# Performance work log

Measured on AMD Instinct MI355X. Metric: run time of the kernel, lower is better.

## Reference

```python
import jax, jax.numpy as jnp
import numpy as np
from jax import lax

H = W = 496
K = 5            # gabor kernel size
WIN = 16         # window_size
STRIDE = 16
PATCH = 32
GAMMA = 0.5
PSI = np.pi / 2
THETAS = np.array([np.pi/8, np.pi/4, 3*np.pi/8, np.pi/2, 5*np.pi/8, 6*np.pi/8, 7*np.pi/8, np.pi], dtype=np.float32)


def setup_inputs() -> dict:
    key = jax.random.key(0)
    k1, k2, k3 = jax.random.split(key, 3)
    img = jax.random.normal(k1, (1, 1, H, W), dtype=jnp.float32)
    sigmas = jax.random.uniform(k2, (1, 3), dtype=jnp.float32) * 10.0   # nn.Parameter(rand*10)
    lambdas = jax.random.uniform(k3, (1, 3), dtype=jnp.float32) * np.pi  # nn.Parameter(rand*pi)
    return {"img": img, "sigmas": sigmas, "lambdas": lambdas}


def _gabor_bank(sigmas, lambdas):
    # axes: (sigma, lambda, theta, ky, kx)
    idx = jnp.arange(K, dtype=jnp.float32) - (K - 1) / 2.0
    sig = sigmas[0][:, None, None, None, None]          # [3,1,1,1,1]
    lam = lambdas[0][None, :, None, None, None]         # [1,3,1,1,1]
    th = jnp.asarray(THETAS)[None, None, :, None, None] # [1,1,8,1,1]
    y = idx[None, None, None, :, None]
    x = idx[None, None, None, None, :]
    sigma_x = sig
    sigma_y = sig / GAMMA
    sin_t, cos_t = jnp.sin(th), jnp.cos(th)
    y_theta = -x * sin_t + y * cos_t
    x_theta = x * cos_t + y * sin_t
    gb = jnp.exp(-0.5 * (x_theta**2 / sigma_x**2 + y_theta**2 / sigma_y**2)) \
         * jnp.cos(2.0 * np.pi * x_theta / lam + PSI)
    return gb.reshape(-1, 1, K, K)  # [72,1,5,5]


def reference(img, sigmas, lambdas):
    gb = _gabor_bank(sigmas, lambdas)
    res = lax.conv_general_dilated(
        img, gb, window_strides=(1, 1), padding=[(K // 2, K // 2)] * 2,
        dimension_numbers=("NCHW", "OIHW", "NCHW"))          # [1,72,H,W]
    res = res.reshape(1, 9, 8, H, W).max(axis=2)              # max over 8 thetas -> [1,9,H,W]
    out = res[0]                                              # [9,H,W]

    # find_maxima: per-channel threshold at 5*mean, zero below (torch.nn.Threshold)
    mean = out.mean(axis=(1, 2), keepdims=True)
    thr = jnp.where(out > mean * 5.0, out, 0.0)

    nw = H // STRIDE                                          # 31
    windows = thr.reshape(9, nw, WIN, nw, WIN).transpose(0, 1, 3, 2, 4).reshape(9, nw * nw, WIN * WIN)
    is_max = jnp.argmax(windows, axis=2) == (WIN * WIN) // 2  # [9, 961]

    w_idx = jnp.arange(nw * nw)
    rows = w_idx // nw * STRIDE + WIN // 2
    cols = w_idx % nw * STRIDE + WIN // 2

    # describe: zero-pad by 16, gather 32x32 patch at each candidate keypoint for every channel
    pad = jnp.pad(out, ((0, 0), (16, 16), (16, 16)))
    pr = rows[:, None, None] + jnp.arange(PATCH)[None, :, None]   # [961,32,1]
    pc = cols[:, None, None] + jnp.arange(PATCH)[None, None, :]   # [961,1,32]
    patches = pad[:, pr, pc]                                      # [9,961,32,32]

    # keep patches only for detected keypoints with nonzero content (original skips zero patches)
    valid_kp = jnp.any(is_max, axis=0)                            # [961]
    nonzero = jnp.any(patches != 0, axis=(2, 3))                  # [9,961]
    mask = (valid_kp[None, :] & nonzero).astype(patches.dtype)
    patches = patches * mask[:, :, None, None]
    return patches
```

## Files before the change

kernel.cpp:

```cpp
#include <hip/hip_runtime.h>
#include <math.h>

#define HH 496
#define WW 496
#define HWSZ (HH*WW)
#define NW 31
#define NWIN (NW*NW)

typedef float nf4 __attribute__((ext_vector_type(4)));

__constant__ float c_thetas[8] = {
    0.39269908169872414f, 0.7853981633974483f, 1.1780972450961724f,
    1.5707963267948966f,  1.9634954084936207f, 2.356194490192345f,
    2.748893571891069f,   3.141592653589793f};

__global__ void bank_kernel(const float* __restrict__ sigmas,
                            const float* __restrict__ lambdas,
                            float* __restrict__ filt,
                            float* __restrict__ meanacc) {
    int idx = threadIdx.x + blockIdx.x * blockDim.x;
    if (idx >= 1800) {
        if (idx < 1809) meanacc[(idx - 1800) * 16] = 0.0f;
        return;
    }
    int f = idx / 25, k = idx % 25;
    int dy = k / 5, dx = k % 5;
    int s = f / 24, rem = f % 24, l = rem / 8, t = rem % 8;
    float sig = sigmas[s], lam = lambdas[l], th = c_thetas[t];
    float y = (float)dy - 2.0f, x = (float)dx - 2.0f;
    float st = sinf(th), ct = cosf(th);
    float yt = -x * st + y * ct;
    float xt =  x * ct + y * st;
    float sx2 = sig * sig;
    float sy2 = 4.0f * sig * sig;
    float g = expf(-0.5f * (xt * xt / sx2 + yt * yt / sy2)) *
              cosf(6.28318530717958647692f * xt / lam + 1.5707963267948966f);
    filt[k * 72 + f] = g;
}

#define FMAS(FP, P) \
    a0  = fmaf(P, (FP)[0],  a0);  a1  = fmaf(P, (FP)[1],  a1);  \
    a2  = fmaf(P, (FP)[2],  a2);  a3  = fmaf(P, (FP)[3],  a3);  \
    a4  = fmaf(P, (FP)[4],  a4);  a5  = fmaf(P, (FP)[5],  a5);  \
    a6  = fmaf(P, (FP)[6],  a6);  a7  = fmaf(P, (FP)[7],  a7);  \
    a8  = fmaf(P, (FP)[8],  a8);  a9  = fmaf(P, (FP)[9],  a9);  \
    a10 = fmaf(P, (FP)[10], a10); a11 = fmaf(P, (FP)[11], a11); \
    a12 = fmaf(P, (FP)[12], a12); a13 = fmaf(P, (FP)[13], a13); \
    a14 = fmaf(P, (FP)[14], a14); a15 = fmaf(P, (FP)[15], a15); \
    a16 = fmaf(P, (FP)[16], a16); a17 = fmaf(P, (FP)[17], a17); \
    a18 = fmaf(P, (FP)[18], a18); a19 = fmaf(P, (FP)[19], a19); \
    a20 = fmaf(P, (FP)[20], a20); a21 = fmaf(P, (FP)[21], a21); \
    a22 = fmaf(P, (FP)[22], a22); a23 = fmaf(P, (FP)[23], a23);

#define STEP(K) { const float* fp = fbase + (K)*72; FMAS(fp, p##K) }

#define ALLSTEPS \
    STEP(0)  STEP(1)  STEP(2)  STEP(3)  STEP(4)  \
    STEP(5)  STEP(6)  STEP(7)  STEP(8)  STEP(9)  \
    STEP(10) STEP(11) STEP(12) STEP(13) STEP(14) \
    STEP(15) STEP(16) STEP(17) STEP(18) STEP(19) \
    STEP(20) STEP(21) STEP(22) STEP(23) STEP(24)

__global__ __launch_bounds__(256) void conv_kernel(
    const float* __restrict__ img, const float* __restrict__ filt,
    float* __restrict__ out, float* __restrict__ meanacc) {
    __shared__ float tile[20 * 20];
    __shared__ float red[4][3];
    int tid = threadIdx.x;
    int tx = tid & 15, ty = tid >> 4;
    int bx = blockIdx.x, by = blockIdx.y, cg = blockIdx.z;

    for (int i = tid; i < 400; i += 256) {
        int tY = i / 20, tX = i % 20;
        int gy = by * 16 + tY - 2, gx = bx * 16 + tX - 2;
        float v = 0.0f;
        if (gy >= 0 && gy < HH && gx >= 0 && gx < WW) v = img[gy * WW + gx];
        tile[i] = v;
    }
    __syncthreads();

    int tbase = ty * 20 + tx;
    float p0  = tile[tbase +  0], p1  = tile[tbase +  1], p2  = tile[tbase +  2],
          p3  = tile[tbase +  3], p4  = tile[tbase +  4];
    float p5  = tile[tbase + 20], p6  = tile[tbase + 21], p7  = tile[tbase + 22],
          p8  = tile[tbase + 23], p9  = tile[tbase + 24];
    float p10 = tile[tbase + 40], p11 = tile[tbase + 41], p12 = tile[tbase + 42],
          p13 = tile[tbase + 43], p14 = tile[tbase + 44];
    float p15 = tile[tbase + 60], p16 = tile[tbase + 61], p17 = tile[tbase + 62],
          p18 = tile[tbase + 63], p19 = tile[tbase + 64];
    float p20 = tile[tbase + 80], p21 = tile[tbase + 81], p22 = tile[tbase + 82],
          p23 = tile[tbase + 83], p24 = tile[tbase + 84];

    float a0=0,a1=0,a2=0,a3=0,a4=0,a5=0,a6=0,a7=0,a8=0,a9=0,a10=0,a11=0,
          a12=0,a13=0,a14=0,a15=0,a16=0,a17=0,a18=0,a19=0,a20=0,a21=0,a22=0,a23=0;
    const float* fbase = filt + cg * 24;

    ALLSTEPS

    int y = by * 16 + ty, x = bx * 16 + tx;

    float m0 = fmaxf(fmaxf(fmaxf(a0,a1),fmaxf(a2,a3)),fmaxf(fmaxf(a4,a5),fmaxf(a6,a7)));
    float m1 = fmaxf(fmaxf(fmaxf(a8,a9),fmaxf(a10,a11)),fmaxf(fmaxf(a12,a13),fmaxf(a14,a15)));
    float m2 = fmaxf(fmaxf(fmaxf(a16,a17),fmaxf(a18,a19)),fmaxf(fmaxf(a20,a21),fmaxf(a22,a23)));

    out[(cg * 3 + 0) * HWSZ + y * WW + x] = m0;
    out[(cg * 3 + 1) * HWSZ + y * WW + x] = m1;
    out[(cg * 3 + 2) * HWSZ + y * WW + x] = m2;

#define RED(CC, MV) { \
        float s = MV; \
        s += __shfl_down(s, 32, 64); s += __shfl_down(s, 16, 64); \
        s += __shfl_down(s,  8, 64); s += __shfl_down(s,  4, 64); \
        s += __shfl_down(s,  2, 64); s += __shfl_down(s,  1, 64); \
        if ((tid & 63) == 0) red[tid >> 6][CC] = s; }
    RED(0, m0) RED(1, m1) RED(2, m2)
    __syncthreads();
    if (tid < 3)
        atomicAdd(&meanacc[(cg * 3 + tid) * 16],
                  red[0][tid] + red[1][tid] + red[2][tid] + red[3][tid]);
}

__global__ __launch_bounds__(256) void patch_kernel(
    const float* __restrict__ out, const float* __restrict__ meanacc,
    float* __restrict__ dst) {
    int w = blockIdx.x;
    int r = w / NW, cl = w % NW;
    int tid = threadIdx.x;
    __shared__ int lds_and[4];
    __shared__ int lds_or[4];

    int wy = tid >> 4, wx = tid & 15;
    int rowbase = (r * 16 + wy) * WW + cl * 16 + wx;
    int cbase   = (r * 16 + 8) * WW + cl * 16;
    int okmask = 0;
#pragma unroll
    for (int c = 0; c < 9; c++) {
        float m5 = meanacc[c * 16] * (5.0f / (float)HWSZ);
        float v  = out[c * HWSZ + rowbase];
        float vc = out[c * HWSZ + cbase];
        float thr  = (v  > m5) ? v  : 0.0f;
        float thrc = (vc > m5) ? vc : 0.0f;
        bool ok = (tid < 128) ? (thr < thrc) : (thr <= thrc);
        okmask |= (ok ? 1 : 0) << c;
    }
#pragma unroll
    for (int off = 1; off < 64; off <<= 1) okmask &= __shfl_xor(okmask, off, 64);
    if ((tid & 63) == 0) lds_and[tid >> 6] = okmask;

    int i = tid >> 3;
    int jg = (tid & 7) << 2;
    int row = r * 16 + i - 8;
    int col = cl * 16 + jg - 8;
    bool inb = (row >= 0 && row < HH && col >= 0 && col + 3 < WW);
    size_t pbase = (size_t)row * WW + col;
    int nzmask = 0;
    nf4 p0, p1, p2, p3, p4, p5, p6, p7, p8;
#define LOADP(C, V) { \
        V = (nf4){0.f, 0.f, 0.f, 0.f}; \
        if (inb) V = *(const nf4*)(out + (size_t)(C) * HWSZ + pbase); \
        if (V.x != 0.f || V.y != 0.f || V.z != 0.f || V.w != 0.f) nzmask |= 1 << (C); }
    LOADP(0,p0) LOADP(1,p1) LOADP(2,p2) LOADP(3,p3) LOADP(4,p4)
    LOADP(5,p5) LOADP(6,p6) LOADP(7,p7) LOADP(8,p8)

#pragma unroll
    for (int off = 1; off < 64; off <<= 1) nzmask |= __shfl_xor(nzmask, off, 64);
    if ((tid & 63) == 0) lds_or[tid >> 6] = nzmask;
    __syncthreads();

    int am = lds_and[0] & lds_and[1] & lds_and[2] & lds_and[3];
    int om = lds_or[0] | lds_or[1] | lds_or[2] | lds_or[3];
    bool valid = (am != 0);

    size_t dbase = (size_t)w * 1024 + i * 32 + jg;
#define STOREP(C, V) { \
        float mk = (valid && ((om >> (C)) & 1)) ? 1.0f : 0.0f; \
        V *= mk; \
        __builtin_nontemporal_store(V, (nf4*)(dst + (size_t)(C) * NWIN * 1024 + dbase)); }
    STOREP(0,p0) STOREP(1,p1) STOREP(2,p2) STOREP(3,p3) STOREP(4,p4)
    STOREP(5,p5) STOREP(6,p6) STOREP(7,p7) STOREP(8,p8)
}

extern "C" void kernel_launch(void* const* d_in, const int* in_sizes, int n_in,
                              void* d_out, int out_size, void* d_ws, size_t ws_size,
                              hipStream_t stream) {
    const float* img     = (const float*)d_in[0];
    const float* sigmas  = (const float*)d_in[1];
    const float* lambdas = (const float*)d_in[2];
    float* ws = (float*)d_ws;
    float* filt    = ws;
    float* meanacc = ws + 2048;
    float* outb    = ws + 4096;

    bank_kernel<<<8, 256, 0, stream>>>(sigmas, lambdas, filt, meanacc);
    conv_kernel<<<dim3(NW, NW, 3), 256, 0, stream>>>(img, filt, outb, meanacc);
    patch_kernel<<<NWIN, 256, 0, stream>>>(outb, meanacc, (float*)d_out);
}
```

Measured before the change: 121.6 us.

## Compute per-window max statistics in conv kernel to simplify keypoint test

The conv kernel now also reduces each 16x16 window to a max over pixels before the centre, a max over pixels after it, and the centre value, and writes these to a small workspace array. The patch kernel decides whether a keypoint is valid from these three values and the channel mean, instead of reloading the whole window per channel and doing a ballot-style reduction. This removes 9 window reads and a cross-wave reduction from the patch kernel. In exchange the conv kernel does an extra max reduction and more shared-memory work. The threshold-then-argmax semantics now rely on comparing the centre against the other maxima without zeroing sub-threshold values, which may behave differently in edge cases.

After: 123.9 us. Within noise of the previous version (+1.9%).

```diff
diff --git a/kernel.cpp b/kernel.cpp
--- a/kernel.cpp
+++ b/kernel.cpp
@@ -1,5 +1,6 @@
 #include <hip/hip_runtime.h>
 #include <math.h>
+#include <float.h>
 
 #define HH 496
 #define WW 496
@@ -63,9 +64,12 @@
 
 __global__ __launch_bounds__(256) void conv_kernel(
     const float* __restrict__ img, const float* __restrict__ filt,
-    float* __restrict__ out, float* __restrict__ meanacc) {
+    float* __restrict__ out, float* __restrict__ meanacc,
+    float* __restrict__ winfo) {
     __shared__ float tile[20 * 20];
     __shared__ float red[4][3];
+    __shared__ float wmax[4][3];
+    __shared__ float cen[3];
     int tid = threadIdx.x;
     int tx = tid & 15, ty = tid >> 4;
     int bx = blockIdx.x, by = blockIdx.y, cg = blockIdx.z;
@@ -107,45 +111,47 @@
     out[(cg * 3 + 1) * HWSZ + y * WW + x] = m1;
     out[(cg * 3 + 2) * HWSZ + y * WW + x] = m2;
 
-#define RED(CC, MV) { \
+#define REDBOTH(CC, MV) { \
         float s = MV; \
         s += __shfl_down(s, 32, 64); s += __shfl_down(s, 16, 64); \
         s += __shfl_down(s,  8, 64); s += __shfl_down(s,  4, 64); \
         s += __shfl_down(s,  2, 64); s += __shfl_down(s,  1, 64); \
-        if ((tid & 63) == 0) red[tid >> 6][CC] = s; }
-    RED(0, m0) RED(1, m1) RED(2, m2)
+        float q = (tid == 128) ? -FLT_MAX : MV; \
+        q = fmaxf(q, __shfl_down(q, 32, 64)); q = fmaxf(q, __shfl_down(q, 16, 64)); \
+        q = fmaxf(q, __shfl_down(q,  8, 64)); q = fmaxf(q, __shfl_down(q,  4, 64)); \
+        q = fmaxf(q, __shfl_down(q,  2, 64)); q = fmaxf(q, __shfl_down(q,  1, 64)); \
+        if ((tid & 63) == 0) { red[tid >> 6][CC] = s; wmax[tid >> 6][CC] = q; } \
+        if (tid == 128) cen[CC] = MV; }
+    REDBOTH(0, m0) REDBOTH(1, m1) REDBOTH(2, m2)
     __syncthreads();
-    if (tid < 3)
+    int w = by * NW + bx;
+    if (tid < 3) {
         atomicAdd(&meanacc[(cg * 3 + tid) * 16],
                   red[0][tid] + red[1][tid] + red[2][tid] + red[3][tid]);
+        int c = cg * 3 + tid;
+        winfo[0 * 9 * NWIN + c * NWIN + w] = fmaxf(wmax[0][tid], wmax[1][tid]);
+        winfo[1 * 9 * NWIN + c * NWIN + w] = fmaxf(wmax[2][tid], wmax[3][tid]);
+        winfo[2 * 9 * NWIN + c * NWIN + w] = cen[tid];
+    }
 }
 
 __global__ __launch_bounds__(256) void patch_kernel(
     const float* __restrict__ out, const float* __restrict__ meanacc,
-    float* __restrict__ dst) {
+    const float* __restrict__ winfo, float* __restrict__ dst) {
     int w = blockIdx.x;
     int r = w / NW, cl = w % NW;
     int tid = threadIdx.x;
-    __shared__ int lds_and[4];
     __shared__ int lds_or[4];
 
-    int wy = tid >> 4, wx = tid & 15;
-    int rowbase = (r * 16 + wy) * WW + cl * 16 + wx;
-    int cbase   = (r * 16 + 8) * WW + cl * 16;
-    int okmask = 0;
+    bool valid = false;
 #pragma unroll
     for (int c = 0; c < 9; c++) {
-        float m5 = meanacc[c * 16] * (5.0f / (float)HWSZ);
-        float v  = out[c * HWSZ + rowbase];
-        float vc = out[c * HWSZ + cbase];
-        float thr  = (v  > m5) ? v  : 0.0f;
-        float thrc = (vc > m5) ? vc : 0.0f;
-        bool ok = (tid < 128) ? (thr < thrc) : (thr <= thrc);
-        okmask |= (ok ? 1 : 0) << c;
-    }
-#pragma unroll
-    for (int off = 1; off < 64; off <<= 1) okmask &= __shfl_xor(okmask, off, 64);
-    if ((tid & 63) == 0) lds_and[tid >> 6] = okmask;
+        float m5  = meanacc[c * 16] * (5.0f / (float)HWSZ);
+        float me  = winfo[0 * 9 * NWIN + c * NWIN + w];
+        float mlt = winfo[1 * 9 * NWIN + c * NWIN + w];
+        float ce  = winfo[2 * 9 * NWIN + c * NWIN + w];
+        if (ce > m5 && ce > me && ce >= mlt) valid = true;
+    }
 
     int i = tid >> 3;
     int jg = (tid & 7) << 2;
@@ -167,9 +173,7 @@
     if ((tid & 63) == 0) lds_or[tid >> 6] = nzmask;
     __syncthreads();
 
-    int am = lds_and[0] & lds_and[1] & lds_and[2] & lds_and[3];
     int om = lds_or[0] | lds_or[1] | lds_or[2] | lds_or[3];
-    bool valid = (am != 0);
 
     size_t dbase = (size_t)w * 1024 + i * 32 + jg;
 #define STOREP(C, V) { \
@@ -189,9 +193,10 @@
     float* ws = (float*)d_ws;
     float* filt    = ws;
     float* meanacc = ws + 2048;
-    float* outb    = ws + 4096;
+    float* winfo   = ws + 2240;
+    float* outb    = ws + 28672;
 
     bank_kernel<<<8, 256, 0, stream>>>(sigmas, lambdas, filt, meanacc);
-    conv_kernel<<<dim3(NW, NW, 3), 256, 0, stream>>>(img, filt, outb, meanacc);
-    patch_kernel<<<NWIN, 256, 0, stream>>>(outb, meanacc, (float*)d_out);
-}
+    conv_kernel<<<dim3(NW, NW, 3), 256, 0, stream>>>(img, filt, outb, meanacc, winfo);
+    patch_kernel<<<NWIN, 256, 0, stream>>>(outb, meanacc, winfo, (float*)d_out);
+}
```
